# Kernel tuning notes

Measured on AMD Instinct MI355X. Metric: run time of the kernel, lower is better.

## Reference

```python
import jax, jax.numpy as jnp
import numpy as np

NUM_HEADS = 16
D_MODEL = 1024
DEPTH = D_MODEL // NUM_HEADS


def rope_sincos(seq_len, depth):
    # standard RoPE: inv_freq over even dims, sin/cos tiled to full depth
    inv_freq = 1.0 / (10000.0 ** (jnp.arange(0, depth, 2, dtype=jnp.float32) / depth))
    ang = jnp.arange(seq_len, dtype=jnp.float32)[:, None] * inv_freq[None, :]  # [S, depth/2]
    sin = jnp.concatenate([jnp.sin(ang), jnp.sin(ang)], axis=-1)  # [S, depth]
    cos = jnp.concatenate([jnp.cos(ang), jnp.cos(ang)], axis=-1)
    return sin, cos


def apply_rope(x, sin, cos):
    # x: [B,H,S,depth]; rotate-half formulation
    half = x.shape[-1] // 2
    x1, x2 = x[..., :half], x[..., half:]
    rot = jnp.concatenate([-x2, x1], axis=-1)
    return x * cos + rot * sin


def setup_inputs() -> dict:
    key = jax.random.key(0)
    ks = jax.random.split(key, 5)
    s = 1.0 / np.sqrt(D_MODEL)
    return {
        "x": jax.random.normal(ks[0], (2, 2048, D_MODEL), dtype=jnp.float32),
        "wq": jax.random.normal(ks[1], (D_MODEL, D_MODEL), dtype=jnp.float32) * s,
        "bq": jnp.zeros((D_MODEL,), jnp.float32),
        "wk": jax.random.normal(ks[2], (D_MODEL, D_MODEL), dtype=jnp.float32) * s,
        "bk": jnp.zeros((D_MODEL,), jnp.float32),
        "wv": jax.random.normal(ks[3], (D_MODEL, D_MODEL), dtype=jnp.float32) * s,
        "bv": jnp.zeros((D_MODEL,), jnp.float32),
        "wo": jax.random.normal(ks[4], (D_MODEL, D_MODEL), dtype=jnp.float32) * s,
        "bo": jnp.zeros((D_MODEL,), jnp.float32),
    }


def reference(x, wq, bq, wk, bk, wv, bv, wo, bo):
    B, S, _ = x.shape

    def split_heads(t):  # [B,S,D] -> [B,H,S,depth]
        return t.reshape(B, S, NUM_HEADS, DEPTH).transpose(0, 2, 1, 3)

    Q = split_heads(x @ wq + bq)
    K = split_heads(x @ wk + bk)
    V = split_heads(x @ wv + bv)

    sin, cos = rope_sincos(S, DEPTH)  # [S, depth], broadcasts over B,H
    Q = apply_rope(Q, sin, cos)
    K = apply_rope(K, sin, cos)

    scores = jnp.einsum("bhqd,bhkd->bhqk", Q, K) / jnp.sqrt(jnp.float32(DEPTH))
    weights = jax.nn.softmax(scores, axis=-1)
    out = jnp.einsum("bhqk,bhkd->bhqd", weights, V)
    out = out.transpose(0, 2, 1, 3).reshape(B, S, D_MODEL)
    return out @ wo + bo
```

## Files before the change

### kernel.cpp

```cpp
#include <hip/hip_runtime.h>

#define DM 1024
#define SEQ 2048
#define NH 16
#define DH 64
#define BATCH 2

typedef _Float16 half_t;
typedef _Float16 half8 __attribute__((ext_vector_type(8)));
typedef _Float16 half4 __attribute__((ext_vector_type(4)));
typedef __fp16 f16x2 __attribute__((ext_vector_type(2)));
typedef unsigned u32x2 __attribute__((ext_vector_type(2)));
typedef unsigned u32x4 __attribute__((ext_vector_type(4)));
typedef float f32x4 __attribute__((ext_vector_type(4)));

__device__ __forceinline__ f32x4 mfma16(half8 a, half8 b, f32x4 c) {
  return __builtin_amdgcn_mfma_f32_16x16x32_f16(a, b, c, 0, 0, 0);
}
__device__ __forceinline__ f32x4 mfma16k16(half4 a, half4 b, f32x4 c) {
  return __builtin_amdgcn_mfma_f32_16x16x16f16(a, b, c, 0, 0, 0);
}

__device__ __forceinline__ void gl2lds16(const half_t* g, half_t* l) {
  __builtin_amdgcn_global_load_lds((const __attribute__((address_space(1))) void*)g,
                                   (__attribute__((address_space(3))) void*)l, 16, 0, 0);
}


__global__ void cvt_x_kernel(const float* __restrict__ x, half_t* __restrict__ xh) {
  int i = (blockIdx.x * 256 + threadIdx.x) * 4;
  float4 v = *(const float4*)(x + i);
  half4 h = { (half_t)v.x, (half_t)v.y, (half_t)v.z, (half_t)v.w };
  *(half4*)(xh + i) = h;
}

__global__ void wtrans_kernel(const float* __restrict__ w0, const float* __restrict__ w1,
                              const float* __restrict__ w2, const float* __restrict__ w3,
                              half_t* __restrict__ o0, half_t* __restrict__ o1,
                              half_t* __restrict__ o2, half_t* __restrict__ o3) {
  __shared__ float tile[32][33];
  const float* w = (blockIdx.z == 0) ? w0 : (blockIdx.z == 1) ? w1 : (blockIdx.z == 2) ? w2 : w3;
  half_t* o = (blockIdx.z == 0) ? o0 : (blockIdx.z == 1) ? o1 : (blockIdx.z == 2) ? o2 : o3;
  int tx = threadIdx.x, ty0 = threadIdx.y;
  int bx = blockIdx.x * 32, by = blockIdx.y * 32;
#pragma unroll
  for (int i = 0; i < 4; i++) {
    int ty = ty0 + i * 8;
    tile[ty][tx] = w[(size_t)(by + ty) * DM + bx + tx];
  }
  __syncthreads();
#pragma unroll
  for (int i = 0; i < 4; i++) {
    int ty = ty0 + i * 8;
    o[(size_t)(bx + ty) * DM + by + tx] = (half_t)tile[tx][ty];
  }
}

__global__ void ropetab_kernel(float* __restrict__ st, float* __restrict__ ct) {
  int idx = blockIdx.x * 256 + threadIdx.x;
  int s = idx >> 5, i = idx & 31;
  float freq = exp2f(-(float)i * (13.287712379549449f / 32.0f));
  float ang = (float)s * freq;
  st[idx] = sinf(ang);
  ct[idx] = cosf(ang);
}


__global__ __launch_bounds__(256)
void qkv_kernel(const half_t* __restrict__ xh,
                const half_t* __restrict__ wtq, const half_t* __restrict__ wtk,
                const half_t* __restrict__ wtv,
                const float* __restrict__ bq, const float* __restrict__ bk,
                const float* __restrict__ bv,
                const float* __restrict__ st, const float* __restrict__ ctab,
                half_t* __restrict__ Qh, half_t* __restrict__ Kh, half_t* __restrict__ Vt) {
  const int tid = threadIdx.x;
  const int wid = tid >> 6, lane = tid & 63;
  const int l16 = lane & 15, quad = lane >> 4;
  const int m0 = blockIdx.y * 128, n0 = blockIdx.x * 128;
  const int g = blockIdx.z;
  const half_t* wt = (g == 0) ? wtq : (g == 1) ? wtk : wtv;
  const float* bias = (g == 0) ? bq : (g == 1) ? bk : bv;
  __shared__ __align__(16) char smem[32768];
  half_t* As = (half_t*)smem;
  half_t* Bs = (half_t*)(smem + 8192);
  f32x4 acc[4][4] = {};
  const int wrow = (wid >> 1) * 64, wcol = (wid & 1) * 64;

  const int ar0 = tid >> 2,          ab0 = (tid & 3) ^ ((ar0 >> 1) & 3);
  const int ar1 = (tid + 256) >> 2,  ab1 = (tid & 3) ^ ((ar1 >> 1) & 3);
  const int swz = (l16 >> 1) & 3;

  for (int k0 = 0; k0 < DM; k0 += 32) {
    __syncthreads();
    gl2lds16(&xh[(size_t)(m0 + ar0) * DM + k0 + ab0 * 8], &As[tid * 8]);
    gl2lds16(&xh[(size_t)(m0 + ar1) * DM + k0 + ab1 * 8], &As[(tid + 256) * 8]);
    gl2lds16(&wt[(size_t)(n0 + ar0) * DM + k0 + ab0 * 8], &Bs[tid * 8]);
    gl2lds16(&wt[(size_t)(n0 + ar1) * DM + k0 + ab1 * 8], &Bs[(tid + 256) * 8]);
    __syncthreads();
    half8 a[4], b[4];
#pragma unroll
    for (int rt = 0; rt < 4; rt++)
      a[rt] = *(const half8*)&As[((wrow + rt * 16 + l16) * 4 + (quad ^ swz)) * 8];
#pragma unroll
    for (int ct = 0; ct < 4; ct++)
      b[ct] = *(const half8*)&Bs[((wcol + ct * 16 + l16) * 4 + (quad ^ swz)) * 8];
#pragma unroll
    for (int rt = 0; rt < 4; rt++)
#pragma unroll
      for (int ct = 0; ct < 4; ct++)
        acc[rt][ct] = mfma16(a[rt], b[ct], acc[rt][ct]);
  }

  const int h = (n0 + wcol) >> 6;
  const float qscale = 0.125f * 1.44269504089f;
  float bv4[4];
#pragma unroll
  for (int ct = 0; ct < 4; ct++) bv4[ct] = bias[n0 + wcol + ct * 16 + l16];

  if (g == 2) {
    __syncthreads();
    half_t* vt = (half_t*)(smem + wid * 8192);
#pragma unroll
    for (int rt = 0; rt < 4; rt++)
#pragma unroll
      for (int ct = 0; ct < 4; ct++) {
        half4 hv;
#pragma unroll
        for (int r = 0; r < 4; r++) hv[r] = (half_t)(acc[rt][ct][r] + bv4[ct]);
        int row = ct * 16 + l16;
        int colu = rt * 2 + (quad >> 1);
        *(half4*)&vt[row * 64 + ((colu ^ (row & 7)) * 8) + (quad & 1) * 4] = hv;
      }
    const int sb = m0 + wrow;
    const int bb = sb >> 11, s0 = sb & 2047;
    half_t* dstv = Vt + (size_t)(bb * NH + h) * DH * SEQ;
#pragma unroll
    for (int i = 0; i < 8; i++) {
      int d = i * 8 + (lane >> 3), c = lane & 7;
      half8 v = *(const half8*)&vt[d * 64 + ((c ^ (d & 7)) * 8)];
      *(half8*)&dstv[(size_t)d * SEQ + s0 + c * 8] = v;
    }
  } else {
    half_t* dst = (g == 0) ? Qh : Kh;
#pragma unroll
    for (int rt = 0; rt < 4; rt++) {
#pragma unroll
      for (int r = 0; r < 4; r++) {
        int m = m0 + wrow + rt * 16 + quad * 4 + r;
        int bb = m >> 11, s = m & 2047;
        float v0 = acc[rt][0][r] + bv4[0];
        float v1 = acc[rt][1][r] + bv4[1];
        float v2 = acc[rt][2][r] + bv4[2];
        float v3 = acc[rt][3][r] + bv4[3];
        float sn0 = st[s * 32 + l16], cs0 = ctab[s * 32 + l16];
        float sn1 = st[s * 32 + 16 + l16], cs1 = ctab[s * 32 + 16 + l16];
        float o0 = v0 * cs0 - v2 * sn0;
        float o1 = v1 * cs1 - v3 * sn1;
        float o2 = v2 * cs0 + v0 * sn0;
        float o3 = v3 * cs1 + v1 * sn1;
        if (g == 0) { o0 *= qscale; o1 *= qscale; o2 *= qscale; o3 *= qscale; }
        size_t base = ((size_t)(bb * NH + h) * SEQ + s) * DH;
        dst[base + l16]      = (half_t)o0;
        dst[base + 16 + l16] = (half_t)o1;
        dst[base + 32 + l16] = (half_t)o2;
        dst[base + 48 + l16] = (half_t)o3;
      }
    }
  }
}


__global__ __launch_bounds__(512)
void attn_kernel(const half_t* __restrict__ Qh, const half_t* __restrict__ Kh,
                 const half_t* __restrict__ Vt, half_t* __restrict__ AO) {
  const int tid = threadIdx.x;
  const int wid = tid >> 6, lane = tid & 63;
  const int l16 = lane & 15, quad = lane >> 4;
  const int lid = blockIdx.x;
  const int bh = lid & 31, qt = lid >> 5;
  const int bb = bh >> 4, h = bh & 15;
  const int q0 = qt * 256 + wid * 32;
  const half_t* Q = Qh + (size_t)bh * SEQ * DH;
  const half_t* K = Kh + (size_t)bh * SEQ * DH;
  const half_t* V = Vt + (size_t)bh * DH * SEQ;
  __shared__ __align__(16) half_t Ks[2][64 * 64];
  __shared__ __align__(16) half_t Vs[2][64 * 64];

  const int r0 = tid >> 3, c0 = (tid & 7) ^ (r0 & 7);
  const int sw0 = ((quad ^ (l16 & 7)) * 8);
  const int sw1 = (((quad + 4) ^ (l16 & 7)) * 8);

  const half_t* gK0 = &K[(size_t)r0 * DH + c0 * 8];
  const half_t* gV0 = &V[(size_t)r0 * SEQ + c0 * 8];

  half8 aqA[2], aqB[2];
#pragma unroll
  for (int rt = 0; rt < 2; rt++) {
    aqA[rt] = *(const half8*)&Q[(size_t)(q0 + rt * 16 + l16) * DH + quad * 8];
    aqB[rt] = *(const half8*)&Q[(size_t)(q0 + rt * 16 + l16) * DH + 32 + quad * 8];
  }

  f32x4 o[2][4] = {};
  f32x4 vsum[2] = {};
  const f32x4 cinit = {-12.f, -12.f, -12.f, -12.f};

  gl2lds16(gK0, &Ks[0][tid * 8]);
  gl2lds16(gV0, &Vs[0][tid * 8]);
  __syncthreads();

  int cur = 0;
  for (int kb0 = 0; kb0 < SEQ; kb0 += 64) {
    const bool pf = (kb0 + 64 < SEQ);
    u32x4 rk0, rv0;
    if (pf) {
      const int kb = kb0 + 64;
      rk0 = *(const u32x4*)(gK0 + (size_t)kb * DH);
      rv0 = *(const u32x4*)(gV0 + kb);
    }
    const half_t* ksrc = Ks[cur];
    const half_t* vsrc = Vs[cur];

    f32x4 z[2][4];
    __builtin_amdgcn_s_setprio(1);
#pragma unroll
    for (int kt = 0; kt < 4; kt++) {
      const half_t* krow = &ksrc[(kt * 16 + l16) * 64];
      half8 b0 = *(const half8*)&krow[sw0];
      half8 b1 = *(const half8*)&krow[sw1];
#pragma unroll
      for (int rt = 0; rt < 2; rt++) {
        f32x4 zz = cinit;
        zz = mfma16(b0, aqA[rt], zz);
        zz = mfma16(b1, aqB[rt], zz);
        z[rt][kt] = zz;
      }
    }
    __builtin_amdgcn_s_setprio(0);

    half4 pa[2][4];
#pragma unroll
    for (int rt = 0; rt < 2; rt++)
#pragma unroll
      for (int kt = 0; kt < 4; kt++) {
        f32x4 p;
#pragma unroll
        for (int r = 0; r < 4; r++) p[r] = __builtin_amdgcn_exp2f(z[rt][kt][r]);
        vsum[rt] += p;
        f16x2 lo = __builtin_amdgcn_cvt_pkrtz(p[0], p[1]);
        f16x2 hi = __builtin_amdgcn_cvt_pkrtz(p[2], p[3]);
        u32x2 w = { __builtin_bit_cast(unsigned, lo), __builtin_bit_cast(unsigned, hi) };
        pa[rt][kt] = __builtin_bit_cast(half4, w);
      }

    __builtin_amdgcn_s_setprio(1);
#pragma unroll
    for (int dt = 0; dt < 4; dt++) {
      const int row = dt * 16 + l16;
      const half_t* vrow = &vsrc[row * 64 + (quad & 1) * 4];
#pragma unroll
      for (int kt = 0; kt < 4; kt++) {
        half4 bv = *(const half4*)&vrow[((kt * 2 + (quad >> 1)) ^ (l16 & 7)) * 8];
#pragma unroll
        for (int rt = 0; rt < 2; rt++)
          o[rt][dt] = mfma16k16(pa[rt][kt], bv, o[rt][dt]);
      }
    }
    __builtin_amdgcn_s_setprio(0);

    if (pf) {
      const int nxt = cur ^ 1;
      *(u32x4*)&Ks[nxt][tid * 8] = rk0;
      *(u32x4*)&Vs[nxt][tid * 8] = rv0;
    }
    __syncthreads();
    cur ^= 1;
  }

  float linv[2][4];
#pragma unroll
  for (int rt = 0; rt < 2; rt++) {
    float s = (vsum[rt][0] + vsum[rt][1]) + (vsum[rt][2] + vsum[rt][3]);
    s += __shfl_xor(s, 16);
    s += __shfl_xor(s, 32);
#pragma unroll
    for (int r = 0; r < 4; r++) linv[rt][r] = 1.f / __shfl(s, quad * 4 + r);
  }
#pragma unroll
  for (int rt = 0; rt < 2; rt++)
#pragma unroll
    for (int dt = 0; dt < 4; dt++)
#pragma unroll
      for (int r = 0; r < 4; r++) {
        int srow = q0 + rt * 16 + quad * 4 + r;
        AO[((size_t)bb * SEQ + srow) * DM + h * DH + dt * 16 + l16] =
            (half_t)(o[rt][dt][r] * linv[rt][r]);
      }
}


__global__ __launch_bounds__(256)
void out_kernel(const half_t* __restrict__ AO, const half_t* __restrict__ wto,
                const float* __restrict__ bo, float* __restrict__ out) {
  const int tid = threadIdx.x;
  const int wid = tid >> 6, lane = tid & 63;
  const int l16 = lane & 15, quad = lane >> 4;
  const int m0 = blockIdx.y * 128, n0 = blockIdx.x * 64;
  __shared__ __align__(16) half_t As[128 * 32];
  __shared__ __align__(16) half_t Bs[64 * 32];
  f32x4 acc[4][2] = {};
  const int wrow = (wid >> 1) * 64, wcol = (wid & 1) * 32;

  const int ar0 = tid >> 2,         ab0 = (tid & 3) ^ ((ar0 >> 1) & 3);
  const int ar1 = (tid + 256) >> 2, ab1 = (tid & 3) ^ ((ar1 >> 1) & 3);
  const int swz = (l16 >> 1) & 3;

  for (int k0 = 0; k0 < DM; k0 += 32) {
    __syncthreads();
    gl2lds16(&AO[(size_t)(m0 + ar0) * DM + k0 + ab0 * 8], &As[tid * 8]);
    gl2lds16(&AO[(size_t)(m0 + ar1) * DM + k0 + ab1 * 8], &As[(tid + 256) * 8]);
    gl2lds16(&wto[(size_t)(n0 + ar0) * DM + k0 + ab0 * 8], &Bs[tid * 8]);
    __syncthreads();
    half8 a[4], b[2];
#pragma unroll
    for (int rt = 0; rt < 4; rt++)
      a[rt] = *(const half8*)&As[((wrow + rt * 16 + l16) * 4 + (quad ^ swz)) * 8];
#pragma unroll
    for (int ct = 0; ct < 2; ct++)
      b[ct] = *(const half8*)&Bs[((wcol + ct * 16 + l16) * 4 + (quad ^ swz)) * 8];
#pragma unroll
    for (int rt = 0; rt < 4; rt++)
#pragma unroll
      for (int ct = 0; ct < 2; ct++)
        acc[rt][ct] = mfma16(a[rt], b[ct], acc[rt][ct]);
  }
  float bv2[2];
#pragma unroll
  for (int ct = 0; ct < 2; ct++) bv2[ct] = bo[n0 + wcol + ct * 16 + l16];
#pragma unroll
  for (int rt = 0; rt < 4; rt++)
#pragma unroll
    for (int r = 0; r < 4; r++) {
      int m = m0 + wrow + rt * 16 + quad * 4 + r;
#pragma unroll
      for (int ct = 0; ct < 2; ct++)
        out[(size_t)m * DM + n0 + wcol + ct * 16 + l16] = acc[rt][ct][r] + bv2[ct];
    }
}


extern "C" void kernel_launch(void* const* d_in, const int* in_sizes, int n_in,
                              void* d_out, int out_size, void* d_ws, size_t ws_size,
                              hipStream_t stream) {
  (void)in_sizes; (void)n_in; (void)out_size; (void)ws_size;
  const float* x  = (const float*)d_in[0];
  const float* wq = (const float*)d_in[1];
  const float* bq = (const float*)d_in[2];
  const float* wk = (const float*)d_in[3];
  const float* bk = (const float*)d_in[4];
  const float* wv = (const float*)d_in[5];
  const float* bv = (const float*)d_in[6];
  const float* wo = (const float*)d_in[7];
  const float* bo = (const float*)d_in[8];
  char* ws = (char*)d_ws;
  const size_t MB = 1u << 20;
  half_t* xh  = (half_t*)(ws + 0);
  half_t* AO  = (half_t*)(ws + 0);
  half_t* wtq = (half_t*)(ws + 8 * MB);
  half_t* wtk = (half_t*)(ws + 10 * MB);
  half_t* wtv = (half_t*)(ws + 12 * MB);
  half_t* wto = (half_t*)(ws + 14 * MB);
  float*  st  = (float*)(ws + 16 * MB);
  float*  ctb = (float*)(ws + 16 * MB + 256 * 1024);
  half_t* Qh  = (half_t*)(ws + 17 * MB);
  half_t* Kh  = (half_t*)(ws + 25 * MB);
  half_t* Vt  = (half_t*)(ws + 33 * MB);
  float* out = (float*)d_out;

  cvt_x_kernel<<<4096, 256, 0, stream>>>(x, xh);
  wtrans_kernel<<<dim3(32, 32, 4), dim3(32, 8), 0, stream>>>(wq, wk, wv, wo, wtq, wtk, wtv, wto);
  ropetab_kernel<<<256, 256, 0, stream>>>(st, ctb);
  qkv_kernel<<<dim3(8, 32, 3), 256, 0, stream>>>(xh, wtq, wtk, wtv, bq, bk, bv, st, ctb, Qh, Kh, Vt);
  attn_kernel<<<256, 512, 0, stream>>>(Qh, Kh, Vt, AO);
  out_kernel<<<dim3(16, 32), 256, 0, stream>>>(AO, wto, bo, out);
}
```

Baseline: 201.9 us.

## Double-buffer LDS tiles in QKV and output projection GEMMs

Both projection GEMM kernels now keep two LDS buffers for the A and B tiles. The next k-tile is prefetched with global_load_lds while MFMAs run on the current tile, so one barrier per iteration replaces the previous pair. The goal is to hide global-to-LDS latency behind matrix compute. LDS use in the output kernel rises to 24 KB, and correctness relies on the barrier waiting for the outstanding async loads before the buffer swap.

```diff
diff --git a/kernel.cpp b/kernel.cpp
--- a/kernel.cpp
+++ b/kernel.cpp
@@ -82,8 +82,6 @@
   const half_t* wt = (g == 0) ? wtq : (g == 1) ? wtk : wtv;
   const float* bias = (g == 0) ? bq : (g == 1) ? bk : bv;
   __shared__ __align__(16) char smem[32768];
-  half_t* As = (half_t*)smem;
-  half_t* Bs = (half_t*)(smem + 8192);
   f32x4 acc[4][4] = {};
   const int wrow = (wid >> 1) * 64, wcol = (wid & 1) * 64;
 
@@ -91,25 +89,43 @@
   const int ar1 = (tid + 256) >> 2,  ab1 = (tid & 3) ^ ((ar1 >> 1) & 3);
   const int swz = (l16 >> 1) & 3;
 
+  {
+    half_t* As = (half_t*)smem;
+    half_t* Bs = (half_t*)(smem + 16384);
+    gl2lds16(&xh[(size_t)(m0 + ar0) * DM + ab0 * 8], &As[tid * 8]);
+    gl2lds16(&xh[(size_t)(m0 + ar1) * DM + ab1 * 8], &As[(tid + 256) * 8]);
+    gl2lds16(&wt[(size_t)(n0 + ar0) * DM + ab0 * 8], &Bs[tid * 8]);
+    gl2lds16(&wt[(size_t)(n0 + ar1) * DM + ab1 * 8], &Bs[(tid + 256) * 8]);
+  }
+  __syncthreads();
+
+  int cur = 0;
   for (int k0 = 0; k0 < DM; k0 += 32) {
-    __syncthreads();
-    gl2lds16(&xh[(size_t)(m0 + ar0) * DM + k0 + ab0 * 8], &As[tid * 8]);
-    gl2lds16(&xh[(size_t)(m0 + ar1) * DM + k0 + ab1 * 8], &As[(tid + 256) * 8]);
-    gl2lds16(&wt[(size_t)(n0 + ar0) * DM + k0 + ab0 * 8], &Bs[tid * 8]);
-    gl2lds16(&wt[(size_t)(n0 + ar1) * DM + k0 + ab1 * 8], &Bs[(tid + 256) * 8]);
-    __syncthreads();
+    if (k0 + 32 < DM) {
+      half_t* Asn = (half_t*)(smem + (cur ^ 1) * 8192);
+      half_t* Bsn = (half_t*)(smem + 16384 + (cur ^ 1) * 8192);
+      const int kn = k0 + 32;
+      gl2lds16(&xh[(size_t)(m0 + ar0) * DM + kn + ab0 * 8], &Asn[tid * 8]);
+      gl2lds16(&xh[(size_t)(m0 + ar1) * DM + kn + ab1 * 8], &Asn[(tid + 256) * 8]);
+      gl2lds16(&wt[(size_t)(n0 + ar0) * DM + kn + ab0 * 8], &Bsn[tid * 8]);
+      gl2lds16(&wt[(size_t)(n0 + ar1) * DM + kn + ab1 * 8], &Bsn[(tid + 256) * 8]);
+    }
+    const half_t* Asc = (const half_t*)(smem + cur * 8192);
+    const half_t* Bsc = (const half_t*)(smem + 16384 + cur * 8192);
     half8 a[4], b[4];
 #pragma unroll
     for (int rt = 0; rt < 4; rt++)
-      a[rt] = *(const half8*)&As[((wrow + rt * 16 + l16) * 4 + (quad ^ swz)) * 8];
+      a[rt] = *(const half8*)&Asc[((wrow + rt * 16 + l16) * 4 + (quad ^ swz)) * 8];
 #pragma unroll
     for (int ct = 0; ct < 4; ct++)
-      b[ct] = *(const half8*)&Bs[((wcol + ct * 16 + l16) * 4 + (quad ^ swz)) * 8];
+      b[ct] = *(const half8*)&Bsc[((wcol + ct * 16 + l16) * 4 + (quad ^ swz)) * 8];
 #pragma unroll
     for (int rt = 0; rt < 4; rt++)
 #pragma unroll
       for (int ct = 0; ct < 4; ct++)
         acc[rt][ct] = mfma16(a[rt], b[ct], acc[rt][ct]);
+    __syncthreads();
+    cur ^= 1;
   }
 
   const int h = (n0 + wcol) >> 6;
@@ -119,7 +135,6 @@
   for (int ct = 0; ct < 4; ct++) bv4[ct] = bias[n0 + wcol + ct * 16 + l16];
 
   if (g == 2) {
-    __syncthreads();
     half_t* vt = (half_t*)(smem + wid * 8192);
 #pragma unroll
     for (int rt = 0; rt < 4; rt++)
@@ -306,8 +321,7 @@
   const int wid = tid >> 6, lane = tid & 63;
   const int l16 = lane & 15, quad = lane >> 4;
   const int m0 = blockIdx.y * 128, n0 = blockIdx.x * 64;
-  __shared__ __align__(16) half_t As[128 * 32];
-  __shared__ __align__(16) half_t Bs[64 * 32];
+  __shared__ __align__(16) char smem[24576];
   f32x4 acc[4][2] = {};
   const int wrow = (wid >> 1) * 64, wcol = (wid & 1) * 32;
 
@@ -315,24 +329,41 @@
   const int ar1 = (tid + 256) >> 2, ab1 = (tid & 3) ^ ((ar1 >> 1) & 3);
   const int swz = (l16 >> 1) & 3;
 
+  {
+    half_t* As = (half_t*)smem;
+    half_t* Bs = (half_t*)(smem + 16384);
+    gl2lds16(&AO[(size_t)(m0 + ar0) * DM + ab0 * 8], &As[tid * 8]);
+    gl2lds16(&AO[(size_t)(m0 + ar1) * DM + ab1 * 8], &As[(tid + 256) * 8]);
+    gl2lds16(&wto[(size_t)(n0 + ar0) * DM + ab0 * 8], &Bs[tid * 8]);
+  }
+  __syncthreads();
+
+  int cur = 0;
   for (int k0 = 0; k0 < DM; k0 += 32) {
-    __syncthreads();
-    gl2lds16(&AO[(size_t)(m0 + ar0) * DM + k0 + ab0 * 8], &As[tid * 8]);
-    gl2lds16(&AO[(size_t)(m0 + ar1) * DM + k0 + ab1 * 8], &As[(tid + 256) * 8]);
-    gl2lds16(&wto[(size_t)(n0 + ar0) * DM + k0 + ab0 * 8], &Bs[tid * 8]);
-    __syncthreads();
+    if (k0 + 32 < DM) {
+      half_t* Asn = (half_t*)(smem + (cur ^ 1) * 8192);
+      half_t* Bsn = (half_t*)(smem + 16384 + (cur ^ 1) * 4096);
+      const int kn = k0 + 32;
+      gl2lds16(&AO[(size_t)(m0 + ar0) * DM + kn + ab0 * 8], &Asn[tid * 8]);
+      gl2lds16(&AO[(size_t)(m0 + ar1) * DM + kn + ab1 * 8], &Asn[(tid + 256) * 8]);
+      gl2lds16(&wto[(size_t)(n0 + ar0) * DM + kn + ab0 * 8], &Bsn[tid * 8]);
+    }
+    const half_t* Asc = (const half_t*)(smem + cur * 8192);
+    const half_t* Bsc = (const half_t*)(smem + 16384 + cur * 4096);
     half8 a[4], b[2];
 #pragma unroll
     for (int rt = 0; rt < 4; rt++)
-      a[rt] = *(const half8*)&As[((wrow + rt * 16 + l16) * 4 + (quad ^ swz)) * 8];
+      a[rt] = *(const half8*)&Asc[((wrow + rt * 16 + l16) * 4 + (quad ^ swz)) * 8];
 #pragma unroll
     for (int ct = 0; ct < 2; ct++)
-      b[ct] = *(const half8*)&Bs[((wcol + ct * 16 + l16) * 4 + (quad ^ swz)) * 8];
+      b[ct] = *(const half8*)&Bsc[((wcol + ct * 16 + l16) * 4 + (quad ^ swz)) * 8];
 #pragma unroll
     for (int rt = 0; rt < 4; rt++)
 #pragma unroll
       for (int ct = 0; ct < 2; ct++)
         acc[rt][ct] = mfma16(a[rt], b[ct], acc[rt][ct]);
+    __syncthreads();
+    cur ^= 1;
   }
   float bv2[2];
 #pragma unroll
```

Measured after the change: 194.1 us. -3.9%, faster.
